# Optimization experiments

Measured on AMD Instinct MI355X. Metric: run time of the kernel, lower is better.

Reference implementation:

```python
import jax, jax.numpy as jnp
import numpy as np
import math

B, T, D = 2, 2048, 1024
H = 16
HD = D // H
DFF = 4096
EPS = 1e-5


def setup_inputs() -> dict:
    key = jax.random.key(0)
    ks = jax.random.split(key, 11)
    s = 0.02
    return {
        "x": jax.random.normal(ks[0], (B, T, D), dtype=jnp.float32),
        "scale1": jnp.ones((D,), jnp.float32),
        "scale2": jnp.ones((D,), jnp.float32),
        "Wqkv": jax.random.normal(ks[1], (D, 3 * D), jnp.float32) * s,
        "bqkv": jnp.zeros((3 * D,), jnp.float32),
        "Wo": jax.random.normal(ks[2], (D, D), jnp.float32) * s,
        "bo": jnp.zeros((D,), jnp.float32),
        "W1": jax.random.normal(ks[3], (D, DFF), jnp.float32) * s,
        "b1": jnp.zeros((DFF,), jnp.float32),
        "W2": jax.random.normal(ks[4], (DFF, D), jnp.float32) * s,
        "b2": jnp.zeros((D,), jnp.float32),
    }


def rmsnorm(x, scale):
    # Faithful to source: norm = ||x||/sqrt(d); out = scale * x / (norm + eps)
    d = x.shape[-1]
    norm = jnp.linalg.norm(x, axis=-1, keepdims=True) * (1.0 / math.sqrt(d))
    return scale * x / (norm + EPS)


def attention(x, Wqkv, bqkv, Wo, bo):
    b, t, c = x.shape
    qkv = x @ Wqkv + bqkv                       # [B,T,3D]
    qkv = qkv.reshape(b, t, 3, H, HD)
    q, k, v = qkv[:, :, 0], qkv[:, :, 1], qkv[:, :, 2]   # [B,T,H,HD]
    scores = jnp.einsum("bqhd,bkhd->bhqk", q, k) / math.sqrt(HD)
    w = jax.nn.softmax(scores, axis=-1)
    out = jnp.einsum("bhqk,bkhd->bqhd", w, v).reshape(b, t, c)
    return out @ Wo + bo


def reference(x, scale1, scale2, Wqkv, bqkv, Wo, bo, W1, b1, W2, b2):
    x = x + attention(rmsnorm(x, scale1), Wqkv, bqkv, Wo, bo)
    h = rmsnorm(x, scale2)
    ff = (jax.nn.gelu(h @ W1 + b1, approximate=False)) @ W2 + b2
    return x + ff
```

## Files before the change

kernel.cpp:

```cpp
#include <hip/hip_runtime.h>
#include <hip/hip_bf16.h>
#include <math.h>

typedef unsigned short u16;
typedef __bf16 bf16x8 __attribute__((ext_vector_type(8)));
typedef float f32x4 __attribute__((ext_vector_type(4)));
typedef unsigned int u32x2 __attribute__((ext_vector_type(2)));

#define B_   2
#define T_   2048
#define D_   1024
#define H_   16
#define HD_  64
#define DFF_ 4096
#define M_TOK (B_*T_)

__device__ __forceinline__ u16 f2bf(float f){
  unsigned u = __float_as_uint(f);
  u += 0x7fff + ((u>>16)&1);
  return (u16)(u>>16);
}
__device__ __forceinline__ float bflo(unsigned u){ return __uint_as_float(u<<16); }
__device__ __forceinline__ float bfhi(unsigned u){ return __uint_as_float(u & 0xffff0000u); }

__device__ __forceinline__ void gl2lds16(const void* g, void* l){
  __builtin_amdgcn_global_load_lds((const __attribute__((address_space(1))) void*)g,
                                   (__attribute__((address_space(3))) void*)l, 16, 0, 0);
}

__device__ __forceinline__ unsigned lds_u32(const void* p){
  return (unsigned)(uintptr_t)(const __attribute__((address_space(3))) void*)p;
}

__device__ __forceinline__ u32x2 tr_read(unsigned addr){
  u32x2 d;
  asm volatile("ds_read_b64_tr_b16 %0, %1" : "=v"(d) : "v"(addr));
  return d;
}
__device__ __forceinline__ u32x2 tr_read512(unsigned addr){
  u32x2 d;
  asm volatile("ds_read_b64_tr_b16 %0, %1 offset:512" : "=v"(d) : "v"(addr));
  return d;
}
__device__ __forceinline__ bf16x8 pack8(u32x2 a, u32x2 b){
  union { u32x2 u[2]; bf16x8 v; } x; x.u[0]=a; x.u[1]=b; return x.v;
}
__device__ __forceinline__ unsigned cvt_pk_bf16(float a, float b){
  unsigned r;
  asm("v_cvt_pk_bf16_f32 %0, %1, %2" : "=v"(r) : "v"(a), "v"(b));
  return r;
}

__device__ __forceinline__ void block_barrier(){
  asm volatile("" ::: "memory");
  __builtin_amdgcn_s_barrier();
  __builtin_amdgcn_sched_barrier(0);
  asm volatile("" ::: "memory");
}

__device__ __forceinline__ int xcd_chunk(int orig, int nwg){
  int q = nwg >> 3, r = nwg & 7;
  int x = orig & 7, s = orig >> 3;
  return (x < r ? x*(q+1) : r*(q+1) + (x-r)*q) + s;
}

__global__ __launch_bounds__(256) void k_transpose_bf16(const float* __restrict__ in,
                                                        u16* __restrict__ out, int K, int N){
  __shared__ float t[32][33];
  int bx = blockIdx.x*32, by = blockIdx.y*32;
  int tx = threadIdx.x, ty = threadIdx.y;
  #pragma unroll
  for(int i=ty;i<32;i+=8) t[i][tx] = in[(size_t)(by+i)*N + bx + tx];
  __syncthreads();
  #pragma unroll
  for(int i=ty;i<32;i+=8) out[(size_t)(bx+i)*K + by + tx] = f2bf(t[tx][i]);
}

__global__ __launch_bounds__(256) void k_rmsnorm_bf16(const float* __restrict__ x,
                                                      const float* __restrict__ scale,
                                                      u16* __restrict__ out){
  int row = blockIdx.x;
  int tid = threadIdx.x;
  int lane = tid&63, wave = tid>>6;
  const float4* xr = (const float4*)(x + (size_t)row*D_);
  float4 v = xr[tid];
  float ss = v.x*v.x + v.y*v.y + v.z*v.z + v.w*v.w;
  #pragma unroll
  for(int o=1;o<64;o<<=1) ss += __shfl_xor(ss, o);
  __shared__ float red[4];
  if(lane==0) red[wave]=ss;
  __syncthreads();
  float tot = red[0]+red[1]+red[2]+red[3];
  float inv = 1.0f/(sqrtf(tot*(1.0f/D_)) + 1e-5f);
  const float4* sr = (const float4*)scale;
  float4 s4 = sr[tid];
  u16* o4 = out + (size_t)row*D_ + tid*4;
  o4[0]=f2bf(v.x*s4.x*inv); o4[1]=f2bf(v.y*s4.y*inv);
  o4[2]=f2bf(v.z*s4.z*inv); o4[3]=f2bf(v.w*s4.w*inv);
}

template<int EPI>
__global__ __launch_bounds__(512,2) void k_gemm256(const u16* __restrict__ A, const u16* __restrict__ Bt,
                                                   const float* __restrict__ bias,
                                                   void* __restrict__ Cout, int M, int N, int K, int nbx){
  __shared__ u16 LDS[4][16384];
  const int tid = threadIdx.x;
  const int lane = tid&63, wave = tid>>6;
  const int lo = lane&15, hi = lane>>4;
  const int wm = wave>>2, wn = wave&3;
  const int l = xcd_chunk(blockIdx.x, gridDim.x);
  const int row0 = (l % nbx)*256, col0 = (l / nbx)*256;
  f32x4 acc[8][4];
  #pragma unroll
  for(int m=0;m<8;m++)
    #pragma unroll
    for(int n=0;n<4;n++) acc[m][n] = (f32x4){0.f,0.f,0.f,0.f};
  const u16* Ag = A + (size_t)row0*K;
  const u16* Bg = Bt + (size_t)col0*K;
  const int NT = K>>5;

  const int cc0 = tid, cc1 = tid+512;
  const size_t s0 = (size_t)(cc0>>2)*K + (size_t)((((cc0&3)^((cc0>>3)&3)))<<3);
  const size_t s1 = (size_t)(cc1>>2)*K + (size_t)((((cc1&3)^((cc1>>3)&3)))<<3);

  #define STAGE_A(t) { const u16* Ab = Ag + (size_t)(t)*32; char* d = (char*)LDS[(t)&3]; \
    gl2lds16(Ab + s0, d + cc0*16); gl2lds16(Ab + s1, d + cc1*16); }
  #define STAGE_B(t) { const u16* Bb = Bg + (size_t)(t)*32; char* d = (char*)LDS[(t)&3] + 16384; \
    gl2lds16(Bb + s0, d + cc0*16); gl2lds16(Bb + s1, d + cc1*16); }

  STAGE_A(0); STAGE_B(0); STAGE_A(1); STAGE_B(1); STAGE_A(2); STAGE_B(2);

  const unsigned slot = (unsigned)((hi ^ ((lo>>1)&3))<<4);
  for(int t=0;t<NT;t++){
    if(t<NT-2)       { asm volatile("s_waitcnt vmcnt(8)" ::: "memory"); }
    else if(t==NT-2) { asm volatile("s_waitcnt vmcnt(4)" ::: "memory"); }
    else             { asm volatile("s_waitcnt vmcnt(0)" ::: "memory"); }
    block_barrier();
    const char* bufp = (const char*)LDS[t&3];
    const char* ap = bufp + (wm*128 + lo)*64 + slot;
    const char* bp = bufp + 16384 + (wn*64 + lo)*64 + slot;

    if(t+3<NT) STAGE_A(t+3);
    __builtin_amdgcn_sched_barrier(0);
    bf16x8 a0[4], b[4];
    #pragma unroll
    for(int m=0;m<4;m++) a0[m] = *(const bf16x8*)(ap + m*1024);
    #pragma unroll
    for(int n=0;n<4;n++) b[n]  = *(const bf16x8*)(bp + n*1024);
    __builtin_amdgcn_s_setprio(1);
    #pragma unroll
    for(int m=0;m<4;m++)
      #pragma unroll
      for(int n=0;n<4;n++)
        acc[m][n] = __builtin_amdgcn_mfma_f32_16x16x32_bf16(a0[m], b[n], acc[m][n], 0,0,0);
    __builtin_amdgcn_s_setprio(0);

    if(t+3<NT) STAGE_B(t+3);
    __builtin_amdgcn_sched_barrier(0);
    bf16x8 a1[4];
    #pragma unroll
    for(int m=0;m<4;m++) a1[m] = *(const bf16x8*)(ap + 4096 + m*1024);
    __builtin_amdgcn_s_setprio(1);
    #pragma unroll
    for(int m=0;m<4;m++)
      #pragma unroll
      for(int n=0;n<4;n++)
        acc[m+4][n] = __builtin_amdgcn_mfma_f32_16x16x32_bf16(a1[m], b[n], acc[m+4][n], 0,0,0);
    __builtin_amdgcn_s_setprio(0);
  }
  #undef STAGE_A
  #undef STAGE_B

  #pragma unroll
  for(int m=0;m<8;m++){
    #pragma unroll
    for(int n=0;n<4;n++){
      #pragma unroll
      for(int r=0;r<4;r++){
        int row = row0 + wm*128 + m*16 + hi*4 + r;
        int col = col0 + wn*64 + n*16 + lo;
        float v = acc[m][n][r] + bias[col];
        if constexpr(EPI==2){
          v = 0.5f*v*(1.0f + erff(v*0.70710678118f));
        }
        ((u16*)Cout)[(size_t)row*N + col] = f2bf(v);
      }
    }
  }
}

__global__ __launch_bounds__(256) void k_gemm_pk(const u16* __restrict__ A, const u16* __restrict__ Bt,
                                                 u16* __restrict__ P, int M, int N, int K, int splitk){
  __shared__ u16 As[128*32];
  __shared__ u16 Bs[128*32];
  int tid = threadIdx.x;
  int lane = tid&63, wave = tid>>6;
  int lo = lane&15, hi = lane>>4;
  int wr = wave>>1, wc = wave&1;
  const int l = xcd_chunk(blockIdx.x, gridDim.x);
  const int nbx = M>>7, nby = N>>7;
  int row0 = (l % nbx)*128;
  int col0 = ((l / nbx) % nby)*128;
  int kc   = l / (nbx*nby);
  int klen = K/splitk, kbeg = kc*klen;
  f32x4 acc[4][4];
  #pragma unroll
  for(int m=0;m<4;m++)
    #pragma unroll
    for(int n=0;n<4;n++) acc[m][n] = (f32x4){0.f,0.f,0.f,0.f};
  const u16* Ag = A + (size_t)row0*K + kbeg;
  const u16* Bg = Bt + (size_t)col0*K + kbeg;
  const unsigned sw = (unsigned)((hi^((lo>>1)&3))*16);
  for(int k0=0;k0<klen;k0+=32){
    __syncthreads();
    #pragma unroll
    for(int c=tid;c<512;c+=256){
      gl2lds16(Ag + (size_t)(c>>2)*K + k0 + (size_t)(((c&3)^((c>>3)&3))<<3), (char*)As + c*16);
      gl2lds16(Bg + (size_t)(c>>2)*K + k0 + (size_t)(((c&3)^((c>>3)&3))<<3), (char*)Bs + c*16);
    }
    __syncthreads();
    const char* ab = (const char*)As + (wr*64+lo)*64;
    const char* bb = (const char*)Bs + (wc*64+lo)*64;
    bf16x8 a[4], b[4];
    #pragma unroll
    for(int m=0;m<4;m++) a[m] = *(const bf16x8*)(ab + m*1024 + sw);
    #pragma unroll
    for(int n=0;n<4;n++) b[n] = *(const bf16x8*)(bb + n*1024 + sw);
    #pragma unroll
    for(int m=0;m<4;m++)
      #pragma unroll
      for(int n=0;n<4;n++)
        acc[m][n] = __builtin_amdgcn_mfma_f32_16x16x32_bf16(a[m], b[n], acc[m][n], 0,0,0);
  }
  u16* Pk = P + (size_t)kc*M*N;
  #pragma unroll
  for(int m=0;m<4;m++)
    #pragma unroll
    for(int n=0;n<4;n++)
      #pragma unroll
      for(int r=0;r<4;r++){
        int row = row0 + wr*64 + m*16 + hi*4 + r;
        int col = col0 + wc*64 + n*16 + lo;
        Pk[(size_t)row*N + col] = f2bf(acc[m][n][r]);
      }
}

__global__ __launch_bounds__(256) void k_ff2_reduce4(const u16* __restrict__ P,
                                                     const float* __restrict__ bias,
                                                     const float* __restrict__ res,
                                                     float* __restrict__ out){
  const size_t stride8 = (size_t)M_TOK*D_/8;
  size_t idx = (size_t)blockIdx.x*256 + threadIdx.x;
  const uint4* p = (const uint4*)P;
  uint4 q0 = p[idx], q1 = p[idx+stride8], q2 = p[idx+2*stride8], q3 = p[idx+3*stride8];
  size_t base = idx*8;
  const float4* rr = (const float4*)(res + base);
  const float4* bb = (const float4*)(bias + (base & (D_-1)));
  float4 r0 = rr[0], r1 = rr[1];
  float4 b0 = bb[0], b1 = bb[1];
  float4 o0, o1;
  unsigned w;
  w=q0.x; o0.x  = bflo(w); o0.y  = bfhi(w);
  w=q0.y; o0.z  = bflo(w); o0.w  = bfhi(w);
  w=q0.z; o1.x  = bflo(w); o1.y  = bfhi(w);
  w=q0.w; o1.z  = bflo(w); o1.w  = bfhi(w);
  w=q1.x; o0.x += bflo(w); o0.y += bfhi(w);
  w=q1.y; o0.z += bflo(w); o0.w += bfhi(w);
  w=q1.z; o1.x += bflo(w); o1.y += bfhi(w);
  w=q1.w; o1.z += bflo(w); o1.w += bfhi(w);
  w=q2.x; o0.x += bflo(w); o0.y += bfhi(w);
  w=q2.y; o0.z += bflo(w); o0.w += bfhi(w);
  w=q2.z; o1.x += bflo(w); o1.y += bfhi(w);
  w=q2.w; o1.z += bflo(w); o1.w += bfhi(w);
  w=q3.x; o0.x += bflo(w); o0.y += bfhi(w);
  w=q3.y; o0.z += bflo(w); o0.w += bfhi(w);
  w=q3.z; o1.x += bflo(w); o1.y += bfhi(w);
  w=q3.w; o1.z += bflo(w); o1.w += bfhi(w);
  o0.x += b0.x + r0.x; o0.y += b0.y + r0.y; o0.z += b0.z + r0.z; o0.w += b0.w + r0.w;
  o1.x += b1.x + r1.x; o1.y += b1.y + r1.y; o1.z += b1.z + r1.z; o1.w += b1.w + r1.w;
  float4* oo = (float4*)(out + base);
  oo[0] = o0; oo[1] = o1;
}

__global__ __launch_bounds__(256) void k_wo_reduce_rms(const u16* __restrict__ P,
                                                       const float* __restrict__ bo,
                                                       const float* __restrict__ x,
                                                       const float* __restrict__ scale2,
                                                       float* __restrict__ x2,
                                                       u16* __restrict__ xn2){
  int row = blockIdx.x;
  int tid = threadIdx.x;
  int lane = tid&63, wave = tid>>6;
  const uint2* p0 = (const uint2*)(P + (size_t)row*D_);
  const uint2* p1 = (const uint2*)(P + (size_t)M_TOK*D_ + (size_t)row*D_);
  uint2 a = p0[tid], b = p1[tid];
  float4 r = ((const float4*)(x + (size_t)row*D_))[tid];
  float4 bi = ((const float4*)bo)[tid];
  float4 v;
  v.x = bflo(a.x) + bflo(b.x) + bi.x + r.x;
  v.y = bfhi(a.x) + bfhi(b.x) + bi.y + r.y;
  v.z = bflo(a.y) + bflo(b.y) + bi.z + r.z;
  v.w = bfhi(a.y) + bfhi(b.y) + bi.w + r.w;
  ((float4*)(x2 + (size_t)row*D_))[tid] = v;
  float ss = v.x*v.x + v.y*v.y + v.z*v.z + v.w*v.w;
  #pragma unroll
  for(int o=1;o<64;o<<=1) ss += __shfl_xor(ss, o);
  __shared__ float red[4];
  if(lane==0) red[wave]=ss;
  __syncthreads();
  float tot = red[0]+red[1]+red[2]+red[3];
  float inv = 1.0f/(sqrtf(tot*(1.0f/D_)) + 1e-5f);
  float4 s4 = ((const float4*)scale2)[tid];
  u16* o4 = xn2 + (size_t)row*D_ + tid*4;
  o4[0]=f2bf(v.x*s4.x*inv); o4[1]=f2bf(v.y*s4.y*inv);
  o4[2]=f2bf(v.z*s4.z*inv); o4[3]=f2bf(v.w*s4.w*inv);
}

__global__ __launch_bounds__(256,4) void k_attn(const u16* __restrict__ qkv, u16* __restrict__ O){
  __shared__ alignas(16) u16 Ks[2][4096];
  __shared__ alignas(16) u16 Vs[2][4096];
  __shared__ alignas(16) u16 Ps[4][1024];
  const int l = xcd_chunk(blockIdx.x, 1024);
  const int qt = l & 31, bh = l >> 5;
  const int h = bh & 15, b = bh >> 4;
  const int tid = threadIdx.x, lane = tid&63, wave = tid>>6;
  const int lo = lane&15, hi = lane>>4, l7 = lane&7;
  const u16* qkvB = qkv + (size_t)b*T_*3072;
  const int hoff = h*64;
  const float C2 = 0.18033688f;

  const int q0 = qt*64 + wave*16;
  const u16* qp = qkvB + (size_t)(q0+lo)*3072 + hoff + hi*8;
  bf16x8 aq0 = *(const bf16x8*)qp;
  bf16x8 aq1 = *(const bf16x8*)(qp+32);

  size_t sK[2], sV[2];
  {
    int cc[2] = {tid, tid+256};
    #pragma unroll
    for(int i=0;i<2;i++){
      int c = cc[i];
      sK[i] = (size_t)(c>>3)*3072 + 1024 + hoff + (((c&7)^((c>>3)&7))<<3);
      int kv = ((c>>5)<<2) + ((c>>1)&3);
      int d0 = (((c&31)>>3)<<4) | ((c&1)<<3);
      sV[i] = (size_t)kv*3072 + 2048 + hoff + d0;
    }
  }
  const unsigned kb0 = (unsigned)lo*128 + (unsigned)((hi^l7))*16;
  const unsigned kb1 = (unsigned)lo*128 + (unsigned)(((hi|4)^l7))*16;
  const unsigned vtr = (unsigned)hi*1024 + (unsigned)lo*2;
  const unsigned swzQ = (unsigned)(lo&7)<<4;

  f32x4 oac[4];
  #pragma unroll
  for(int n=0;n<4;n++) oac[n] = (f32x4){0.f,0.f,0.f,0.f};
  float mrow = -1e30f;
  float lsum = 0.f;

  {
    char* kd = (char*)Ks[0]; char* vd = (char*)Vs[0];
    gl2lds16(qkvB + sK[0], kd + tid*16);
    gl2lds16(qkvB + sK[1], kd + tid*16 + 4096);
    gl2lds16(qkvB + sV[0], vd + tid*16);
    gl2lds16(qkvB + sV[1], vd + tid*16 + 4096);
  }
  int buf = 0;
  for(int t=0;t<T_/64;t++){
    __syncthreads();
    if(t < T_/64-1){
      size_t koff = (size_t)(t+1)*64*3072;
      char* kd = (char*)Ks[buf^1]; char* vd = (char*)Vs[buf^1];
      gl2lds16(qkvB + koff + sK[0], kd + tid*16);
      gl2lds16(qkvB + koff + sK[1], kd + tid*16 + 4096);
      gl2lds16(qkvB + koff + sV[0], vd + tid*16);
      gl2lds16(qkvB + koff + sV[1], vd + tid*16 + 4096);
    }
    const char* K_ = (const char*)Ks[buf];
    u16* P_ = Ps[wave];

    f32x4 s[4];
    __builtin_amdgcn_s_setprio(1);
    #pragma unroll
    for(int n=0;n<4;n++){
      bf16x8 k0f = *(const bf16x8*)(K_ + n*2048 + kb0);
      bf16x8 k1f = *(const bf16x8*)(K_ + n*2048 + kb1);
      f32x4 z = (f32x4){0.f,0.f,0.f,0.f};
      z = __builtin_amdgcn_mfma_f32_16x16x32_bf16(k0f, aq0, z, 0,0,0);
      z = __builtin_amdgcn_mfma_f32_16x16x32_bf16(k1f, aq1, z, 0,0,0);
      s[n] = z;
    }
    __builtin_amdgcn_s_setprio(0);

    float mx = s[0][0];
    #pragma unroll
    for(int n=0;n<4;n++)
      #pragma unroll
      for(int r=0;r<4;r++) mx = fmaxf(mx, s[n][r]);

    if(!__all(mx <= mrow + 64.0f)){
      float mm = fmaxf(mx, __shfl_xor(mx,16));
      mm = fmaxf(mm, __shfl_xor(mm,32));
      float nm = fmaxf(mrow, mm);
      float alpha = exp2f((mrow - nm)*C2);
      mrow = nm;
      lsum *= alpha;
      float ar[4];
      #pragma unroll
      for(int r=0;r<4;r++) ar[r] = __shfl(alpha, hi*4 + r);
      #pragma unroll
      for(int n=0;n<4;n++)
        #pragma unroll
        for(int r=0;r<4;r++) oac[n][r] *= ar[r];
    }

    const float nmC2 = -mrow*C2;
    #pragma unroll
    for(int n=0;n<4;n++){
      float p0v = exp2f(fmaf(s[n][0], C2, nmC2));
      float p1v = exp2f(fmaf(s[n][1], C2, nmC2));
      float p2v = exp2f(fmaf(s[n][2], C2, nmC2));
      float p3v = exp2f(fmaf(s[n][3], C2, nmC2));
      lsum += (p0v+p1v)+(p2v+p3v);
      u32x2 pw;
      pw[0] = cvt_pk_bf16(p0v, p1v);
      pw[1] = cvt_pk_bf16(p2v, p3v);
      *(u32x2*)((char*)P_ + (unsigned)lo*128 + (((unsigned)(n*32 + hi*8)) ^ swzQ)) = pw;
    }

    const unsigned vsb = lds_u32(Vs[buf]);
    #pragma unroll
    for(int kk=0;kk<2;kk++){
      bf16x8 ap = *(const bf16x8*)((const char*)P_ + (kk==0 ? kb0 : kb1));
      u32x2 t0[4], t1[4];
      #pragma unroll
      for(int n=0;n<4;n++){
        unsigned a = vsb + vtr + (unsigned)kk*4096 + (unsigned)n*128;
        t0[n] = tr_read(a);
        t1[n] = tr_read512(a);
      }
      asm volatile("s_waitcnt lgkmcnt(0)" ::: "memory");
      __builtin_amdgcn_sched_barrier(0);
      __builtin_amdgcn_s_setprio(1);
      #pragma unroll
      for(int n=0;n<4;n++){
        bf16x8 bv = pack8(t0[n], t1[n]);
        oac[n] = __builtin_amdgcn_mfma_f32_16x16x32_bf16(ap, bv, oac[n], 0,0,0);
      }
      __builtin_amdgcn_s_setprio(0);
    }
    buf ^= 1;
  }

  lsum += __shfl_xor(lsum, 16);
  lsum += __shfl_xor(lsum, 32);
  float linv = 1.0f/lsum;
  float lr[4];
  #pragma unroll
  for(int r=0;r<4;r++) lr[r] = __shfl(linv, hi*4 + r);
  size_t obase = ((size_t)b*T_ + q0)*D_ + hoff;
  #pragma unroll
  for(int n=0;n<4;n++)
    #pragma unroll
    for(int r=0;r<4;r++)
      O[obase + (size_t)(hi*4+r)*D_ + n*16 + lo] = f2bf(oac[n][r]*lr[r]);
}

extern "C" void kernel_launch(void* const* d_in, const int* in_sizes, int n_in,
                              void* d_out, int out_size, void* d_ws, size_t ws_size,
                              hipStream_t stream){
  (void)in_sizes; (void)n_in; (void)out_size; (void)ws_size;
  const float* x      = (const float*)d_in[0];
  const float* scale1 = (const float*)d_in[1];
  const float* scale2 = (const float*)d_in[2];
  const float* Wqkv   = (const float*)d_in[3];
  const float* bqkv   = (const float*)d_in[4];
  const float* Wo     = (const float*)d_in[5];
  const float* bo     = (const float*)d_in[6];
  const float* W1     = (const float*)d_in[7];
  const float* b1     = (const float*)d_in[8];
  const float* W2     = (const float*)d_in[9];
  const float* b2     = (const float*)d_in[10];
  float* out = (float*)d_out;

  char* w = (char*)d_ws;
  u16* xn1   = (u16*)w;  w += (size_t)M_TOK*D_*2;
  u16* qkvb  = (u16*)w;  w += (size_t)M_TOK*3*D_*2;
  u16* Obuf  = (u16*)w;  w += (size_t)M_TOK*D_*2;
  float* x2  = (float*)w; w += (size_t)M_TOK*D_*4;
  u16* xn2   = (u16*)w;  w += (size_t)M_TOK*D_*2;
  u16* h1    = (u16*)w;  w += (size_t)M_TOK*DFF_*2;
  u16* Wqkvt = (u16*)w;  w += (size_t)3*D_*D_*2;
  u16* Wot   = (u16*)w;  w += (size_t)D_*D_*2;
  u16* W1t   = (u16*)w;  w += (size_t)D_*DFF_*2;
  u16* W2t   = (u16*)w;  w += (size_t)DFF_*D_*2;
  u16* wop = (u16*)d_ws;
  u16* pkb = (u16*)d_ws;

  dim3 tb(32,8);
  k_transpose_bf16<<<dim3(3*D_/32, D_/32), tb, 0, stream>>>(Wqkv, Wqkvt, D_, 3*D_);
  k_transpose_bf16<<<dim3(D_/32,   D_/32), tb, 0, stream>>>(Wo,   Wot,   D_, D_);
  k_transpose_bf16<<<dim3(DFF_/32, D_/32), tb, 0, stream>>>(W1,   W1t,   D_, DFF_);
  k_transpose_bf16<<<dim3(D_/32, DFF_/32), tb, 0, stream>>>(W2,   W2t,   DFF_, D_);

  k_rmsnorm_bf16<<<M_TOK, 256, 0, stream>>>(x, scale1, xn1);
  k_gemm256<0><<<192, 512, 0, stream>>>(xn1, Wqkvt, bqkv, qkvb, M_TOK, 3*D_, D_, M_TOK/256);
  k_attn<<<1024, 256, 0, stream>>>(qkvb, Obuf);
  k_gemm_pk<<<512, 256, 0, stream>>>(Obuf, Wot, wop, M_TOK, D_, D_, 2);
  k_wo_reduce_rms<<<M_TOK, 256, 0, stream>>>(wop, bo, x, scale2, x2, xn2);
  k_gemm256<2><<<256, 512, 0, stream>>>(xn2, W1t, b1, h1, M_TOK, DFF_, D_, M_TOK/256);
  k_gemm_pk<<<1024, 256, 0, stream>>>(h1, W2t, pkb, M_TOK, D_, DFF_, 4);
  k_ff2_reduce4<<<2048, 256, 0, stream>>>(pkb, b2, x2, out);
}
```

Baseline: 270.3 us.

## Route Wo and FF2 split-K GEMMs through the pipelined 256-tile kernel

Adds split-K support to the 256x256 multi-stage pipelined GEMM kernel and uses it for the Wo projection and the second FFN GEMM, replacing the simpler 128-tile, single-buffered k_gemm_pk kernel. The Wo GEMM moves from split-K 2 to split-K 4, so the reduce+RMSnorm kernel now sums four partials. Larger tiles and the prefetch pipeline should improve data reuse and latency hiding. The cost is fewer blocks per launch (256), more partial-sum traffic for Wo, and short K loops (8 tiles for Wo) where pipeline fill and drain overhead is relatively large.

```diff
diff --git a/kernel.cpp b/kernel.cpp
--- a/kernel.cpp
+++ b/kernel.cpp
@@ -102,22 +102,26 @@
 template<int EPI>
 __global__ __launch_bounds__(512,2) void k_gemm256(const u16* __restrict__ A, const u16* __restrict__ Bt,
                                                    const float* __restrict__ bias,
-                                                   void* __restrict__ Cout, int M, int N, int K, int nbx){
+                                                   void* __restrict__ Cout, int M, int N, int K,
+                                                   int nbx, int nby, int splitk){
   __shared__ u16 LDS[4][16384];
   const int tid = threadIdx.x;
   const int lane = tid&63, wave = tid>>6;
   const int lo = lane&15, hi = lane>>4;
   const int wm = wave>>2, wn = wave&3;
   const int l = xcd_chunk(blockIdx.x, gridDim.x);
-  const int row0 = (l % nbx)*256, col0 = (l / nbx)*256;
+  const int row0 = (l % nbx)*256;
+  const int col0 = ((l / nbx) % nby)*256;
+  const int kc   = l / (nbx*nby);
+  const int klen = K/splitk, kbeg = kc*klen;
   f32x4 acc[8][4];
   #pragma unroll
   for(int m=0;m<8;m++)
     #pragma unroll
     for(int n=0;n<4;n++) acc[m][n] = (f32x4){0.f,0.f,0.f,0.f};
-  const u16* Ag = A + (size_t)row0*K;
-  const u16* Bg = Bt + (size_t)col0*K;
-  const int NT = K>>5;
+  const u16* Ag = A + (size_t)row0*K + kbeg;
+  const u16* Bg = Bt + (size_t)col0*K + kbeg;
+  const int NT = klen>>5;
 
   const int cc0 = tid, cc1 = tid+512;
   const size_t s0 = (size_t)(cc0>>2)*K + (size_t)((((cc0&3)^((cc0>>3)&3)))<<3);
@@ -171,6 +175,7 @@
   #undef STAGE_A
   #undef STAGE_B
 
+  u16* Pk = (u16*)Cout + (size_t)kc*M*N;
   #pragma unroll
   for(int m=0;m<8;m++){
     #pragma unroll
@@ -179,70 +184,18 @@
       for(int r=0;r<4;r++){
         int row = row0 + wm*128 + m*16 + hi*4 + r;
         int col = col0 + wn*64 + n*16 + lo;
-        float v = acc[m][n][r] + bias[col];
-        if constexpr(EPI==2){
-          v = 0.5f*v*(1.0f + erff(v*0.70710678118f));
+        if constexpr(EPI==3){
+          Pk[(size_t)row*N + col] = f2bf(acc[m][n][r]);
+        } else {
+          float v = acc[m][n][r] + bias[col];
+          if constexpr(EPI==2){
+            v = 0.5f*v*(1.0f + erff(v*0.70710678118f));
+          }
+          ((u16*)Cout)[(size_t)row*N + col] = f2bf(v);
         }
-        ((u16*)Cout)[(size_t)row*N + col] = f2bf(v);
       }
     }
   }
-}
-
-__global__ __launch_bounds__(256) void k_gemm_pk(const u16* __restrict__ A, const u16* __restrict__ Bt,
-                                                 u16* __restrict__ P, int M, int N, int K, int splitk){
-  __shared__ u16 As[128*32];
-  __shared__ u16 Bs[128*32];
-  int tid = threadIdx.x;
-  int lane = tid&63, wave = tid>>6;
-  int lo = lane&15, hi = lane>>4;
-  int wr = wave>>1, wc = wave&1;
-  const int l = xcd_chunk(blockIdx.x, gridDim.x);
-  const int nbx = M>>7, nby = N>>7;
-  int row0 = (l % nbx)*128;
-  int col0 = ((l / nbx) % nby)*128;
-  int kc   = l / (nbx*nby);
-  int klen = K/splitk, kbeg = kc*klen;
-  f32x4 acc[4][4];
-  #pragma unroll
-  for(int m=0;m<4;m++)
-    #pragma unroll
-    for(int n=0;n<4;n++) acc[m][n] = (f32x4){0.f,0.f,0.f,0.f};
-  const u16* Ag = A + (size_t)row0*K + kbeg;
-  const u16* Bg = Bt + (size_t)col0*K + kbeg;
-  const unsigned sw = (unsigned)((hi^((lo>>1)&3))*16);
-  for(int k0=0;k0<klen;k0+=32){
-    __syncthreads();
-    #pragma unroll
-    for(int c=tid;c<512;c+=256){
-      gl2lds16(Ag + (size_t)(c>>2)*K + k0 + (size_t)(((c&3)^((c>>3)&3))<<3), (char*)As + c*16);
-      gl2lds16(Bg + (size_t)(c>>2)*K + k0 + (size_t)(((c&3)^((c>>3)&3))<<3), (char*)Bs + c*16);
-    }
-    __syncthreads();
-    const char* ab = (const char*)As + (wr*64+lo)*64;
-    const char* bb = (const char*)Bs + (wc*64+lo)*64;
-    bf16x8 a[4], b[4];
-    #pragma unroll
-    for(int m=0;m<4;m++) a[m] = *(const bf16x8*)(ab + m*1024 + sw);
-    #pragma unroll
-    for(int n=0;n<4;n++) b[n] = *(const bf16x8*)(bb + n*1024 + sw);
-    #pragma unroll
-    for(int m=0;m<4;m++)
-      #pragma unroll
-      for(int n=0;n<4;n++)
-        acc[m][n] = __builtin_amdgcn_mfma_f32_16x16x32_bf16(a[m], b[n], acc[m][n], 0,0,0);
-  }
-  u16* Pk = P + (size_t)kc*M*N;
-  #pragma unroll
-  for(int m=0;m<4;m++)
-    #pragma unroll
-    for(int n=0;n<4;n++)
-      #pragma unroll
-      for(int r=0;r<4;r++){
-        int row = row0 + wr*64 + m*16 + hi*4 + r;
-        int col = col0 + wc*64 + n*16 + lo;
-        Pk[(size_t)row*N + col] = f2bf(acc[m][n][r]);
-      }
 }
 
 __global__ __launch_bounds__(256) void k_ff2_reduce4(const u16* __restrict__ P,
@@ -291,16 +244,19 @@
   int row = blockIdx.x;
   int tid = threadIdx.x;
   int lane = tid&63, wave = tid>>6;
-  const uint2* p0 = (const uint2*)(P + (size_t)row*D_);
-  const uint2* p1 = (const uint2*)(P + (size_t)M_TOK*D_ + (size_t)row*D_);
-  uint2 a = p0[tid], b = p1[tid];
+  const size_t stride = (size_t)M_TOK*D_;
+  const u16* pr = P + (size_t)row*D_;
+  uint2 a0 = ((const uint2*)pr)[tid];
+  uint2 a1 = ((const uint2*)(pr + stride))[tid];
+  uint2 a2 = ((const uint2*)(pr + 2*stride))[tid];
+  uint2 a3 = ((const uint2*)(pr + 3*stride))[tid];
   float4 r = ((const float4*)(x + (size_t)row*D_))[tid];
   float4 bi = ((const float4*)bo)[tid];
   float4 v;
-  v.x = bflo(a.x) + bflo(b.x) + bi.x + r.x;
-  v.y = bfhi(a.x) + bfhi(b.x) + bi.y + r.y;
-  v.z = bflo(a.y) + bflo(b.y) + bi.z + r.z;
-  v.w = bfhi(a.y) + bfhi(b.y) + bi.w + r.w;
+  v.x = bflo(a0.x)+bflo(a1.x)+bflo(a2.x)+bflo(a3.x) + bi.x + r.x;
+  v.y = bfhi(a0.x)+bfhi(a1.x)+bfhi(a2.x)+bfhi(a3.x) + bi.y + r.y;
+  v.z = bflo(a0.y)+bflo(a1.y)+bflo(a2.y)+bflo(a3.y) + bi.z + r.z;
+  v.w = bfhi(a0.y)+bfhi(a1.y)+bfhi(a2.y)+bfhi(a3.y) + bi.w + r.w;
   ((float4*)(x2 + (size_t)row*D_))[tid] = v;
   float ss = v.x*v.x + v.y*v.y + v.z*v.z + v.w*v.w;
   #pragma unroll
@@ -503,11 +459,11 @@
   k_transpose_bf16<<<dim3(D_/32, DFF_/32), tb, 0, stream>>>(W2,   W2t,   DFF_, D_);
 
   k_rmsnorm_bf16<<<M_TOK, 256, 0, stream>>>(x, scale1, xn1);
-  k_gemm256<0><<<192, 512, 0, stream>>>(xn1, Wqkvt, bqkv, qkvb, M_TOK, 3*D_, D_, M_TOK/256);
+  k_gemm256<0><<<192, 512, 0, stream>>>(xn1, Wqkvt, bqkv, qkvb, M_TOK, 3*D_, D_, M_TOK/256, 3*D_/256, 1);
   k_attn<<<1024, 256, 0, stream>>>(qkvb, Obuf);
-  k_gemm_pk<<<512, 256, 0, stream>>>(Obuf, Wot, wop, M_TOK, D_, D_, 2);
+  k_gemm256<3><<<256, 512, 0, stream>>>(Obuf, Wot, nullptr, wop, M_TOK, D_, D_, M_TOK/256, D_/256, 4);
   k_wo_reduce_rms<<<M_TOK, 256, 0, stream>>>(wop, bo, x, scale2, x2, xn2);
-  k_gemm256<2><<<256, 512, 0, stream>>>(xn2, W1t, b1, h1, M_TOK, DFF_, D_, M_TOK/256);
-  k_gemm_pk<<<1024, 256, 0, stream>>>(h1, W2t, pkb, M_TOK, D_, DFF_, 4);
+  k_gemm256<2><<<256, 512, 0, stream>>>(xn2, W1t, b1, h1, M_TOK, DFF_, D_, M_TOK/256, DFF_/256, 1);
+  k_gemm256<3><<<256, 512, 0, stream>>>(h1, W2t, nullptr, pkb, M_TOK, D_, DFF_, M_TOK/256, D_/256, 4);
   k_ff2_reduce4<<<2048, 256, 0, stream>>>(pkb, b2, x2, out);
 }
```

Measured after the change: 260.8 us (median of 2 runs). -3.5%, faster.
